# Performance work log

Hardware: AMD Instinct MI355X
Metric: run time of the kernel (lower is better)

Reference implementation:

```python
import jax, jax.numpy as jnp
import numpy as np

B, S, D, H = 16, 1024, 512, 8
HD = D // H  # head dim = 64
NEG_INF = jnp.float32(-jnp.inf)


def setup_inputs() -> dict:
    key = jax.random.key(0)
    ks = jax.random.split(key, 7)
    s = 0.02
    return {
        "Q": jax.random.normal(ks[0], (B, S, D), dtype=jnp.float32),
        "Wq_w": jax.random.normal(ks[1], (D, D), dtype=jnp.float32) * s,
        "Wq_b": jax.random.normal(ks[2], (D,), dtype=jnp.float32) * s,
        "Wk_w": jax.random.normal(ks[3], (D, D), dtype=jnp.float32) * s,
        "Wk_b": jax.random.normal(ks[4], (D,), dtype=jnp.float32) * s,
        "Wv_w": jax.random.normal(ks[5], (D, D), dtype=jnp.float32) * s,
        "Wv_b": jax.random.normal(ks[6], (D,), dtype=jnp.float32) * s,
        "ln_w": jnp.ones((D,), dtype=jnp.float32),
        "ln_b": jnp.zeros((D,), dtype=jnp.float32),
    }


def _heads(x):  # [B,S,D] -> [B,H,S,HD]
    return x.reshape(B, S, H, HD).transpose(0, 2, 1, 3)


def reference(Q, Wq_w, Wq_b, Wk_w, Wk_b, Wv_w, Wv_b, ln_w, ln_b):
    # row mask: a row is padding iff all features are zero; True in attn_mask = masked
    valid = jnp.any(Q != 0, axis=-1)                      # [B,S]
    attn_mask = ~(valid[:, :, None] & valid[:, None, :])  # [B,S,S], True=masked
    add_mask = jnp.where(attn_mask, NEG_INF, 0.0)[:, None, :, :]  # [B,1,S,S]

    q = jax.nn.relu(Q @ Wq_w.T + Wq_b)
    k = jax.nn.relu(Q @ Wk_w.T + Wk_b)
    v = jax.nn.relu(Q @ Wv_w.T + Wv_b)
    qh, kh, vh = _heads(q), _heads(k), _heads(v)          # [B,H,S,HD]

    scale = 1.0 / np.sqrt(HD)
    scores = jnp.einsum("bhqd,bhkd->bhqk", qh, kh) * scale + add_mask
    w = jax.nn.softmax(scores, axis=-1)
    w = jnp.nan_to_num(w, nan=0.0)  # fully-masked rows -> 0 (matches torch nan_to_num)
    # dropout p=0.0 (eval) -> identity
    attn = jnp.einsum("bhqk,bhkd->bhqd", w, vh)

    out = attn + qh                                       # residual in multiheaded view
    out = out.transpose(0, 2, 1, 3).reshape(B, S, D)      # from_multiheaded

    mu = jnp.mean(out, axis=-1, keepdims=True)
    var = jnp.var(out, axis=-1, keepdims=True)
    out = (out - mu) * jax.lax.rsqrt(var + 1e-5) * ln_w + ln_b
    out = jax.nn.relu(out)

    weights = w.reshape(B * H, S, S)  # matches torch [B*H, S, S]
    return out, weights
```

## Files before the change

### kernel.cpp

```cpp
#include <hip/hip_runtime.h>
#include <stdint.h>

typedef unsigned short u16;
typedef __attribute__((ext_vector_type(8))) __bf16 bf16x8;
typedef __attribute__((ext_vector_type(8))) u16 u16x8;
typedef __attribute__((ext_vector_type(4))) float f32x4;

__device__ __forceinline__ u16 f2bf(float f) {
    unsigned u = __float_as_uint(f);
    u += 0x7fffu + ((u >> 16) & 1u);
    return (u16)(u >> 16);
}
__device__ __forceinline__ float bf2f(u16 h) {
    return __uint_as_float(((unsigned)h) << 16);
}

__global__ void k_prep(const float* __restrict__ Q,
                       const float* __restrict__ Wq, const float* __restrict__ Wk,
                       const float* __restrict__ Wv,
                       u16* __restrict__ qb, u16* __restrict__ wall,
                       float* __restrict__ fmask) {
    int bid = blockIdx.x;
    int t = threadIdx.x;
    if (bid < 16384) {
        const float* src = Q + (size_t)bid * 512;
        u16* dst = qb + (size_t)bid * 512;
        float4 v0 = *(const float4*)(src + t * 4);
        float4 v1 = *(const float4*)(src + 256 + t * 4);
        bool nz = (v0.x != 0.f) || (v0.y != 0.f) || (v0.z != 0.f) || (v0.w != 0.f) ||
                  (v1.x != 0.f) || (v1.y != 0.f) || (v1.z != 0.f) || (v1.w != 0.f);
        ushort4 o0 = make_ushort4(f2bf(v0.x), f2bf(v0.y), f2bf(v0.z), f2bf(v0.w));
        ushort4 o1 = make_ushort4(f2bf(v1.x), f2bf(v1.y), f2bf(v1.z), f2bf(v1.w));
        *(ushort4*)(dst + t * 4) = o0;
        *(ushort4*)(dst + 256 + t * 4) = o1;
        unsigned long long bal = __ballot(nz);
        if (t == 0) fmask[bid] = bal ? 0.0f : -1e30f;
    } else {
        int r = bid - 16384;
        const float* W = (r < 512) ? Wq : (r < 1024) ? Wk : Wv;
        const float* src = W + (size_t)(r & 511) * 512;
        u16* dst = wall + (size_t)r * 512;
        float4 v0 = *(const float4*)(src + t * 4);
        float4 v1 = *(const float4*)(src + 256 + t * 4);
        ushort4 o0 = make_ushort4(f2bf(v0.x), f2bf(v0.y), f2bf(v0.z), f2bf(v0.w));
        ushort4 o1 = make_ushort4(f2bf(v1.x), f2bf(v1.y), f2bf(v1.z), f2bf(v1.w));
        *(ushort4*)(dst + t * 4) = o0;
        *(ushort4*)(dst + 256 + t * 4) = o1;
    }
}

__global__ __launch_bounds__(256) void k_qkv(
        const u16* __restrict__ qb, const u16* __restrict__ wall,
        const float* __restrict__ bq, const float* __restrict__ bk,
        const float* __restrict__ bv,
        u16* __restrict__ oq, u16* __restrict__ ok, u16* __restrict__ vT) {
    __shared__ u16 As[128 * 32];
    __shared__ u16 Bs[128 * 32];
    int bm = blockIdx.x, bn = blockIdx.y;
    int tid = threadIdx.x, lane = tid & 63, wid = tid >> 6;
    int wm = wid >> 1, wn = wid & 1;
    int q4 = lane >> 4, l16 = lane & 15;

    f32x4 acc[4][4];
#pragma unroll
    for (int i = 0; i < 4; ++i)
#pragma unroll
        for (int j = 0; j < 4; ++j) acc[i][j] = (f32x4){0.f, 0.f, 0.f, 0.f};

#pragma unroll 1
    for (int kk = 0; kk < 16; ++kk) {
        float4 av[2], bw[2];
#pragma unroll
        for (int c = 0; c < 2; ++c) {
            int id = c * 256 + tid;
            int r = id >> 2, cb = (id & 3) * 8;
            av[c] = *(const float4*)(qb + ((size_t)(bm * 128 + r)) * 512 + kk * 32 + cb);
            bw[c] = *(const float4*)(wall + ((size_t)(bn * 128 + r)) * 512 + kk * 32 + cb);
        }
        __syncthreads();
#pragma unroll
        for (int c = 0; c < 2; ++c) {
            int id = c * 256 + tid;
            int r = id >> 2, cb = (id & 3) * 8;
            *(float4*)(&As[r * 32 + cb]) = av[c];
            *(float4*)(&Bs[r * 32 + cb]) = bw[c];
        }
        __syncthreads();
        bf16x8 af[4], bf[4];
#pragma unroll
        for (int i = 0; i < 4; ++i)
            af[i] = *(const bf16x8*)(&As[(wm * 64 + i * 16 + l16) * 32 + q4 * 8]);
#pragma unroll
        for (int j = 0; j < 4; ++j)
            bf[j] = *(const bf16x8*)(&Bs[(wn * 64 + j * 16 + l16) * 32 + q4 * 8]);
#pragma unroll
        for (int i = 0; i < 4; ++i)
#pragma unroll
            for (int j = 0; j < 4; ++j)
                acc[i][j] = __builtin_amdgcn_mfma_f32_16x16x32_bf16(af[i], bf[j], acc[i][j], 0, 0, 0);
    }

    int which = bn >> 2;
    if (which < 2) {
        const float* bias = (which == 0) ? bq : bk;
        u16* outp = (which == 0) ? oq : ok;
#pragma unroll
        for (int i = 0; i < 4; ++i)
#pragma unroll
            for (int j = 0; j < 4; ++j) {
                int n = bn * 128 + wn * 64 + j * 16 + l16;
                int c = n & 511;
                float bb = bias[c];
#pragma unroll
                for (int r = 0; r < 4; ++r) {
                    int m = bm * 128 + wm * 64 + i * 16 + q4 * 4 + r;
                    float val = acc[i][j][r] + bb;
                    val = fmaxf(val, 0.f);
                    outp[(size_t)m * 512 + c] = f2bf(val);
                }
            }
    } else {
        size_t vrow0 = (size_t)(bm >> 3) * 512;
        int s0base = ((bm & 7) * 128) + wm * 64;
#pragma unroll
        for (int i = 0; i < 4; ++i)
#pragma unroll
            for (int j = 0; j < 4; ++j) {
                int c = (bn * 128 + wn * 64 + j * 16 + l16) & 511;
                float bb = bv[c];
                ushort4 o;
                o.x = f2bf(fmaxf(acc[i][j][0] + bb, 0.f));
                o.y = f2bf(fmaxf(acc[i][j][1] + bb, 0.f));
                o.z = f2bf(fmaxf(acc[i][j][2] + bb, 0.f));
                o.w = f2bf(fmaxf(acc[i][j][3] + bb, 0.f));
                int s0 = s0base + i * 16 + q4 * 4;
                *(ushort4*)(vT + (vrow0 + c) * 1024 + s0) = o;
            }
    }
}

__global__ __launch_bounds__(256, 1) void k_attn(
        const u16* __restrict__ qv, const u16* __restrict__ kv,
        const u16* __restrict__ vT, const float* __restrict__ fmask,
        float* __restrict__ outAtt, float* __restrict__ outW) {
    extern __shared__ char smem[];
    char* Wsb = smem;
    char* Ksb = smem + 131072;
    char* Vsb = smem + 147456;
    float* linv = (float*)(smem + 131072);

    int bid = blockIdx.x;
    int qt = bid & 15, h = (bid >> 4) & 7, b = bid >> 7;
    int tid = threadIdx.x, lane = tid & 63, w = tid >> 6;
    int q4 = lane >> 4, l16 = lane & 15;
    const float scale = 0.125f;

    size_t qrow0 = (size_t)b * 1024 + qt * 64;
    size_t headcol = (size_t)h * 64;

    const u16* qp = qv + (qrow0 + w * 16 + l16) * 512 + headcol;
    bf16x8 a0 = *(const bf16x8*)(qp + q4 * 8);
    bf16x8 a1 = *(const bf16x8*)(qp + 32 + q4 * 8);

    float qmv[4], lrun[4];
#pragma unroll
    for (int r = 0; r < 4; ++r) {
        qmv[r] = fmask[qrow0 + w * 16 + q4 * 4 + r];
        lrun[r] = 0.f;
    }
    f32x4 accO[4];
#pragma unroll
    for (int jn = 0; jn < 4; ++jn) accO[jn] = (f32x4){0.f, 0.f, 0.f, 0.f};

#pragma unroll 1
    for (int kt = 0; kt < 8; ++kt) {
        size_t krow0 = (size_t)b * 1024 + kt * 128;
        __syncthreads();
#pragma unroll
        for (int c = 0; c < 4; ++c) {
            int id = c * 256 + tid;
            int r = id >> 3, cb = (id & 7) * 8;
            float4 t4 = *(const float4*)(kv + (krow0 + r) * 512 + headcol + cb);
            *(float4*)(Ksb + ((r * 128 + cb * 2) ^ ((r & 7) << 4))) = t4;
        }
#pragma unroll
        for (int c = 0; c < 4; ++c) {
            int id = c * 256 + tid;
            int hd = id >> 4, cb = (id & 15) * 8;
            float4 t4 = *(const float4*)(vT + ((size_t)b * 512 + headcol + hd) * 1024 + kt * 128 + cb);
            *(float4*)(Vsb + ((hd * 256 + cb * 2) ^ ((hd & 7) << 4))) = t4;
        }
        float km[8];
#pragma unroll
        for (int j = 0; j < 8; ++j) km[j] = fmask[krow0 + j * 16 + l16];
        __syncthreads();

        f32x4 acc[8];
#pragma unroll
        for (int j = 0; j < 8; ++j) acc[j] = (f32x4){0.f, 0.f, 0.f, 0.f};
#pragma unroll
        for (int j = 0; j < 8; ++j) {
            int kr = j * 16 + l16;
            bf16x8 b0 = *(const bf16x8*)(Ksb + ((kr * 128 + q4 * 16) ^ ((kr & 7) << 4)));
            bf16x8 b1 = *(const bf16x8*)(Ksb + ((kr * 128 + 64 + q4 * 16) ^ ((kr & 7) << 4)));
            acc[j] = __builtin_amdgcn_mfma_f32_16x16x32_bf16(a0, b0, acc[j], 0, 0, 0);
            acc[j] = __builtin_amdgcn_mfma_f32_16x16x32_bf16(a1, b1, acc[j], 0, 0, 0);
        }
#pragma unroll
        for (int j = 0; j < 8; ++j)
#pragma unroll
            for (int r = 0; r < 4; ++r)
                acc[j][r] = __expf(acc[j][r] * scale + qmv[r] + km[j]);
#pragma unroll
        for (int r = 0; r < 4; ++r) {
            float ps = 0.f;
#pragma unroll
            for (int j = 0; j < 8; ++j) ps += acc[j][r];
#pragma unroll
            for (int mm = 1; mm <= 8; mm <<= 1) ps += __shfl_xor(ps, mm, 64);
            lrun[r] += ps;
        }
        int wrbase = w * 16 + q4 * 4;
#pragma unroll
        for (int j = 0; j < 8; ++j)
#pragma unroll
            for (int r = 0; r < 4; ++r) {
                int row = wrbase + r;
                int boff = (row * 2048 + kt * 256 + j * 32 + l16 * 2) ^ ((row & 7) << 4);
                *(u16*)(Wsb + boff) = f2bf(acc[j][r]);
            }
        int arow = w * 16 + l16;
#pragma unroll
        for (int ks = 0; ks < 4; ++ks) {
            bf16x8 aw = *(const bf16x8*)(Wsb + ((arow * 2048 + kt * 256 + ks * 64 + q4 * 16) ^ ((arow & 7) << 4)));
#pragma unroll
            for (int jn = 0; jn < 4; ++jn) {
                int vrow = jn * 16 + l16;
                bf16x8 bvv = *(const bf16x8*)(Vsb + ((vrow * 256 + ks * 64 + q4 * 16) ^ ((vrow & 7) << 4)));
                accO[jn] = __builtin_amdgcn_mfma_f32_16x16x32_bf16(aw, bvv, accO[jn], 0, 0, 0);
            }
        }
    }

    float rl[4];
#pragma unroll
    for (int r = 0; r < 4; ++r)
        rl[r] = (qmv[r] == 0.f && lrun[r] > 0.f) ? (1.f / lrun[r]) : 0.f;

    __syncthreads();
    if (l16 == 0) {
#pragma unroll
        for (int r = 0; r < 4; ++r) linv[w * 16 + q4 * 4 + r] = rl[r];
    }

#pragma unroll
    for (int jn = 0; jn < 4; ++jn)
#pragma unroll
        for (int r = 0; r < 4; ++r) {
            int rowC = w * 16 + q4 * 4 + r;
            int hd = jn * 16 + l16;
            float qres = bf2f(qv[(qrow0 + rowC) * 512 + headcol + hd]);
            outAtt[(qrow0 + rowC) * 512 + headcol + hd] = accO[jn][r] * rl[r] + qres;
        }
    __syncthreads();

    int row = tid >> 2, cq = tid & 3;
    float rlr = linv[row];
    size_t wbase = (((size_t)(b * 8 + h)) * 1024 + qt * 64 + row) * 1024;
#pragma unroll 4
    for (int ch = 0; ch < 32; ++ch) {
        int col = ch * 32 + cq * 8;
        u16x8 wv = *(const u16x8*)(Wsb + ((row * 2048 + col * 2) ^ ((row & 7) << 4)));
        float4 o0, o1;
        o0.x = bf2f(wv[0]) * rlr;
        o0.y = bf2f(wv[1]) * rlr;
        o0.z = bf2f(wv[2]) * rlr;
        o0.w = bf2f(wv[3]) * rlr;
        o1.x = bf2f(wv[4]) * rlr;
        o1.y = bf2f(wv[5]) * rlr;
        o1.z = bf2f(wv[6]) * rlr;
        o1.w = bf2f(wv[7]) * rlr;
        *(float4*)(outW + wbase + col) = o0;
        *(float4*)(outW + wbase + col + 4) = o1;
    }
}

__global__ void k_ln(float* __restrict__ io, const float* __restrict__ lw,
                     const float* __restrict__ lb) {
    int row = blockIdx.x;
    int t = threadIdx.x;
    float* p = io + (size_t)row * 512;
    float4 x0 = *(const float4*)(p + t * 4);
    float4 x1 = *(const float4*)(p + 256 + t * 4);
    float s = x0.x + x0.y + x0.z + x0.w + x1.x + x1.y + x1.z + x1.w;
    float s2 = x0.x * x0.x + x0.y * x0.y + x0.z * x0.z + x0.w * x0.w +
               x1.x * x1.x + x1.y * x1.y + x1.z * x1.z + x1.w * x1.w;
#pragma unroll
    for (int mm = 1; mm <= 32; mm <<= 1) {
        s += __shfl_xor(s, mm, 64);
        s2 += __shfl_xor(s2, mm, 64);
    }
    float mean = s * (1.f / 512.f);
    float var = s2 * (1.f / 512.f) - mean * mean;
    float inv = rsqrtf(var + 1e-5f);
    float4 w0 = *(const float4*)(lw + t * 4);
    float4 w1 = *(const float4*)(lw + 256 + t * 4);
    float4 b0 = *(const float4*)(lb + t * 4);
    float4 b1 = *(const float4*)(lb + 256 + t * 4);
    float4 o0, o1;
    o0.x = fmaxf((x0.x - mean) * inv * w0.x + b0.x, 0.f);
    o0.y = fmaxf((x0.y - mean) * inv * w0.y + b0.y, 0.f);
    o0.z = fmaxf((x0.z - mean) * inv * w0.z + b0.z, 0.f);
    o0.w = fmaxf((x0.w - mean) * inv * w0.w + b0.w, 0.f);
    o1.x = fmaxf((x1.x - mean) * inv * w1.x + b1.x, 0.f);
    o1.y = fmaxf((x1.y - mean) * inv * w1.y + b1.y, 0.f);
    o1.z = fmaxf((x1.z - mean) * inv * w1.z + b1.z, 0.f);
    o1.w = fmaxf((x1.w - mean) * inv * w1.w + b1.w, 0.f);
    *(float4*)(p + t * 4) = o0;
    *(float4*)(p + 256 + t * 4) = o1;
}

extern "C" void kernel_launch(void* const* d_in, const int* in_sizes, int n_in,
                              void* d_out, int out_size, void* d_ws, size_t ws_size,
                              hipStream_t stream) {
    const float* Q = (const float*)d_in[0];
    const float* Wq_w = (const float*)d_in[1];
    const float* Wq_b = (const float*)d_in[2];
    const float* Wk_w = (const float*)d_in[3];
    const float* Wk_b = (const float*)d_in[4];
    const float* Wv_w = (const float*)d_in[5];
    const float* Wv_b = (const float*)d_in[6];
    const float* ln_w = (const float*)d_in[7];
    const float* ln_b = (const float*)d_in[8];

    u16* ws16 = (u16*)d_ws;
    u16* qb   = ws16;
    u16* wall = ws16 + 8388608;
    u16* oq   = ws16 + 9175040;
    u16* okk  = ws16 + 17563648;
    u16* vT   = ws16 + 25952256;
    float* fmask = (float*)((char*)d_ws + 68681728);

    float* outAtt = (float*)d_out;
    float* outW = (float*)d_out + 8388608;

    static bool s_attr = false;
    if (!s_attr) {
        hipFuncSetAttribute((const void*)k_attn,
                            hipFuncAttributeMaxDynamicSharedMemorySize, 163840);
        s_attr = true;
    }

    k_prep<<<17920, 64, 0, stream>>>(Q, Wq_w, Wk_w, Wv_w, qb, wall, fmask);
    k_qkv<<<dim3(128, 12), 256, 0, stream>>>(qb, wall, Wq_b, Wk_b, Wv_b, oq, okk, vT);
    k_attn<<<2048, 256, 163840, stream>>>(oq, okk, vT, fmask, outAtt, outW);
    k_ln<<<16384, 64, 0, stream>>>(outAtt, ln_w, ln_b);
}
```

Baseline: 883.1 us.

## Restructure attention as two-pass recompute with per-wave LDS for occupancy

The attention kernel drops the 160KB shared buffer that held the full bf16 weight row block plus staged K/V tiles. Each wave now reads K and V^T fragments straight from global memory and keeps only a small per-wave LDS tile for the PV MFMA operand. A second pass recomputes QK^T and exp to write the normalized fp32 weights directly. Launch bounds go to 4 blocks per CU and block indices are swizzled so concurrent blocks share the same batch's K/V in cache. This trades doubled QK^T/exp work and uncached global K/V fragment loads for much higher occupancy and no block-wide syncs.

```diff
diff --git a/kernel.cpp b/kernel.cpp
--- a/kernel.cpp
+++ b/kernel.cpp
@@ -139,26 +139,25 @@
     }
 }
 
-__global__ __launch_bounds__(256, 1) void k_attn(
+__global__ __launch_bounds__(256, 4) void k_attn(
         const u16* __restrict__ qv, const u16* __restrict__ kv,
         const u16* __restrict__ vT, const float* __restrict__ fmask,
         float* __restrict__ outAtt, float* __restrict__ outW) {
-    extern __shared__ char smem[];
-    char* Wsb = smem;
-    char* Ksb = smem + 131072;
-    char* Vsb = smem + 147456;
-    float* linv = (float*)(smem + 131072);
+    __shared__ u16 Ws[4][16 * 136];
 
     int bid = blockIdx.x;
-    int qt = bid & 15, h = (bid >> 4) & 7, b = bid >> 7;
+    int swz = ((bid & 7) << 8) | (bid >> 3);
+    int qt = swz & 15, h = (swz >> 4) & 7, b = swz >> 7;
     int tid = threadIdx.x, lane = tid & 63, w = tid >> 6;
     int q4 = lane >> 4, l16 = lane & 15;
     const float scale = 0.125f;
 
     size_t qrow0 = (size_t)b * 1024 + qt * 64;
-    size_t headcol = (size_t)h * 64;
-
-    const u16* qp = qv + (qrow0 + w * 16 + l16) * 512 + headcol;
+    size_t hc = (size_t)h * 64;
+    size_t krowB = (size_t)b * 1024;
+    u16* wsw = Ws[w];
+
+    const u16* qp = qv + (qrow0 + w * 16 + l16) * 512 + hc;
     bf16x8 a0 = *(const bf16x8*)(qp + q4 * 8);
     bf16x8 a1 = *(const bf16x8*)(qp + 32 + q4 * 8);
 
@@ -172,116 +171,87 @@
 #pragma unroll
     for (int jn = 0; jn < 4; ++jn) accO[jn] = (f32x4){0.f, 0.f, 0.f, 0.f};
 
+    const u16* vbase = vT + ((size_t)b * 512 + hc) * 1024;
+
 #pragma unroll 1
     for (int kt = 0; kt < 8; ++kt) {
-        size_t krow0 = (size_t)b * 1024 + kt * 128;
-        __syncthreads();
-#pragma unroll
-        for (int c = 0; c < 4; ++c) {
-            int id = c * 256 + tid;
-            int r = id >> 3, cb = (id & 7) * 8;
-            float4 t4 = *(const float4*)(kv + (krow0 + r) * 512 + headcol + cb);
-            *(float4*)(Ksb + ((r * 128 + cb * 2) ^ ((r & 7) << 4))) = t4;
-        }
-#pragma unroll
-        for (int c = 0; c < 4; ++c) {
-            int id = c * 256 + tid;
-            int hd = id >> 4, cb = (id & 15) * 8;
-            float4 t4 = *(const float4*)(vT + ((size_t)b * 512 + headcol + hd) * 1024 + kt * 128 + cb);
-            *(float4*)(Vsb + ((hd * 256 + cb * 2) ^ ((hd & 7) << 4))) = t4;
-        }
+        const u16* kbase = kv + (krowB + kt * 128) * 512 + hc;
+        f32x4 acc[8];
         float km[8];
 #pragma unroll
-        for (int j = 0; j < 8; ++j) km[j] = fmask[krow0 + j * 16 + l16];
-        __syncthreads();
-
-        f32x4 acc[8];
-#pragma unroll
         for (int j = 0; j < 8; ++j) acc[j] = (f32x4){0.f, 0.f, 0.f, 0.f};
 #pragma unroll
         for (int j = 0; j < 8; ++j) {
-            int kr = j * 16 + l16;
-            bf16x8 b0 = *(const bf16x8*)(Ksb + ((kr * 128 + q4 * 16) ^ ((kr & 7) << 4)));
-            bf16x8 b1 = *(const bf16x8*)(Ksb + ((kr * 128 + 64 + q4 * 16) ^ ((kr & 7) << 4)));
+            const u16* kr = kbase + (size_t)(j * 16 + l16) * 512;
+            bf16x8 b0 = *(const bf16x8*)(kr + q4 * 8);
+            bf16x8 b1 = *(const bf16x8*)(kr + 32 + q4 * 8);
+            km[j] = fmask[krowB + kt * 128 + j * 16 + l16];
             acc[j] = __builtin_amdgcn_mfma_f32_16x16x32_bf16(a0, b0, acc[j], 0, 0, 0);
             acc[j] = __builtin_amdgcn_mfma_f32_16x16x32_bf16(a1, b1, acc[j], 0, 0, 0);
         }
 #pragma unroll
         for (int j = 0; j < 8; ++j)
 #pragma unroll
-            for (int r = 0; r < 4; ++r)
-                acc[j][r] = __expf(acc[j][r] * scale + qmv[r] + km[j]);
+            for (int r = 0; r < 4; ++r) {
+                float e = __expf(acc[j][r] * scale + qmv[r] + km[j]);
+                lrun[r] += e;
+                wsw[(q4 * 4 + r) * 136 + j * 16 + l16] = f2bf(e);
+            }
+        const u16* vkt = vbase + kt * 128;
+#pragma unroll
+        for (int ks = 0; ks < 4; ++ks) {
+            bf16x8 aw = *(const bf16x8*)(&wsw[l16 * 136 + ks * 32 + q4 * 8]);
+#pragma unroll
+            for (int jn = 0; jn < 4; ++jn) {
+                bf16x8 bvv = *(const bf16x8*)(vkt + (size_t)(jn * 16 + l16) * 1024 + ks * 32 + q4 * 8);
+                accO[jn] = __builtin_amdgcn_mfma_f32_16x16x32_bf16(aw, bvv, accO[jn], 0, 0, 0);
+            }
+        }
+    }
+
+    float rl[4];
+#pragma unroll
+    for (int r = 0; r < 4; ++r) {
+        float s = lrun[r];
+#pragma unroll
+        for (int mm = 1; mm <= 8; mm <<= 1) s += __shfl_xor(s, mm, 64);
+        rl[r] = (qmv[r] == 0.f && s > 0.f) ? (1.f / s) : 0.f;
+    }
+
+#pragma unroll
+    for (int jn = 0; jn < 4; ++jn)
 #pragma unroll
         for (int r = 0; r < 4; ++r) {
-            float ps = 0.f;
-#pragma unroll
-            for (int j = 0; j < 8; ++j) ps += acc[j][r];
-#pragma unroll
-            for (int mm = 1; mm <= 8; mm <<= 1) ps += __shfl_xor(ps, mm, 64);
-            lrun[r] += ps;
-        }
-        int wrbase = w * 16 + q4 * 4;
+            int rowC = q4 * 4 + r;
+            int hd = jn * 16 + l16;
+            float qres = bf2f(qv[(qrow0 + w * 16 + rowC) * 512 + hc + hd]);
+            outAtt[(qrow0 + w * 16 + rowC) * 512 + hc + hd] = accO[jn][r] * rl[r] + qres;
+        }
+
+    size_t wbase = ((size_t)(b * 8 + h)) * 1024 * 1024 + (size_t)(qt * 64 + w * 16) * 1024;
+#pragma unroll 1
+    for (int kt = 0; kt < 8; ++kt) {
+        const u16* kbase = kv + (krowB + kt * 128) * 512 + hc;
+        f32x4 acc[8];
+        float km[8];
+#pragma unroll
+        for (int j = 0; j < 8; ++j) acc[j] = (f32x4){0.f, 0.f, 0.f, 0.f};
+#pragma unroll
+        for (int j = 0; j < 8; ++j) {
+            const u16* kr = kbase + (size_t)(j * 16 + l16) * 512;
+            bf16x8 b0 = *(const bf16x8*)(kr + q4 * 8);
+            bf16x8 b1 = *(const bf16x8*)(kr + 32 + q4 * 8);
+            km[j] = fmask[krowB + kt * 128 + j * 16 + l16];
+            acc[j] = __builtin_amdgcn_mfma_f32_16x16x32_bf16(a0, b0, acc[j], 0, 0, 0);
+            acc[j] = __builtin_amdgcn_mfma_f32_16x16x32_bf16(a1, b1, acc[j], 0, 0, 0);
+        }
 #pragma unroll
         for (int j = 0; j < 8; ++j)
 #pragma unroll
             for (int r = 0; r < 4; ++r) {
-                int row = wrbase + r;
-                int boff = (row * 2048 + kt * 256 + j * 32 + l16 * 2) ^ ((row & 7) << 4);
-                *(u16*)(Wsb + boff) = f2bf(acc[j][r]);
-            }
-        int arow = w * 16 + l16;
-#pragma unroll
-        for (int ks = 0; ks < 4; ++ks) {
-            bf16x8 aw = *(const bf16x8*)(Wsb + ((arow * 2048 + kt * 256 + ks * 64 + q4 * 16) ^ ((arow & 7) << 4)));
-#pragma unroll
-            for (int jn = 0; jn < 4; ++jn) {
-                int vrow = jn * 16 + l16;
-                bf16x8 bvv = *(const bf16x8*)(Vsb + ((vrow * 256 + ks * 64 + q4 * 16) ^ ((vrow & 7) << 4)));
-                accO[jn] = __builtin_amdgcn_mfma_f32_16x16x32_bf16(aw, bvv, accO[jn], 0, 0, 0);
-            }
-        }
-    }
-
-    float rl[4];
-#pragma unroll
-    for (int r = 0; r < 4; ++r)
-        rl[r] = (qmv[r] == 0.f && lrun[r] > 0.f) ? (1.f / lrun[r]) : 0.f;
-
-    __syncthreads();
-    if (l16 == 0) {
-#pragma unroll
-        for (int r = 0; r < 4; ++r) linv[w * 16 + q4 * 4 + r] = rl[r];
-    }
-
-#pragma unroll
-    for (int jn = 0; jn < 4; ++jn)
-#pragma unroll
-        for (int r = 0; r < 4; ++r) {
-            int rowC = w * 16 + q4 * 4 + r;
-            int hd = jn * 16 + l16;
-            float qres = bf2f(qv[(qrow0 + rowC) * 512 + headcol + hd]);
-            outAtt[(qrow0 + rowC) * 512 + headcol + hd] = accO[jn][r] * rl[r] + qres;
-        }
-    __syncthreads();
-
-    int row = tid >> 2, cq = tid & 3;
-    float rlr = linv[row];
-    size_t wbase = (((size_t)(b * 8 + h)) * 1024 + qt * 64 + row) * 1024;
-#pragma unroll 4
-    for (int ch = 0; ch < 32; ++ch) {
-        int col = ch * 32 + cq * 8;
-        u16x8 wv = *(const u16x8*)(Wsb + ((row * 2048 + col * 2) ^ ((row & 7) << 4)));
-        float4 o0, o1;
-        o0.x = bf2f(wv[0]) * rlr;
-        o0.y = bf2f(wv[1]) * rlr;
-        o0.z = bf2f(wv[2]) * rlr;
-        o0.w = bf2f(wv[3]) * rlr;
-        o1.x = bf2f(wv[4]) * rlr;
-        o1.y = bf2f(wv[5]) * rlr;
-        o1.z = bf2f(wv[6]) * rlr;
-        o1.w = bf2f(wv[7]) * rlr;
-        *(float4*)(outW + wbase + col) = o0;
-        *(float4*)(outW + wbase + col + 4) = o1;
+                float e = __expf(acc[j][r] * scale + qmv[r] + km[j]) * rl[r];
+                outW[wbase + (size_t)(q4 * 4 + r) * 1024 + kt * 128 + j * 16 + l16] = e;
+            }
     }
 }
 
@@ -344,15 +314,8 @@
     float* outAtt = (float*)d_out;
     float* outW = (float*)d_out + 8388608;
 
-    static bool s_attr = false;
-    if (!s_attr) {
-        hipFuncSetAttribute((const void*)k_attn,
-                            hipFuncAttributeMaxDynamicSharedMemorySize, 163840);
-        s_attr = true;
-    }
-
     k_prep<<<17920, 64, 0, stream>>>(Q, Wq_w, Wk_w, Wv_w, qb, wall, fmask);
     k_qkv<<<dim3(128, 12), 256, 0, stream>>>(qb, wall, Wq_b, Wk_b, Wv_b, oq, okk, vT);
-    k_attn<<<2048, 256, 163840, stream>>>(oq, okk, vT, fmask, outAtt, outW);
+    k_attn<<<2048, 256, 0, stream>>>(oq, okk, vT, fmask, outAtt, outW);
     k_ln<<<16384, 64, 0, stream>>>(outAtt, ln_w, ln_b);
 }
```

Result: slower. 1.036 ms (+17.3%).
